# Optimization experiments

Hardware: AMD Instinct MI355X
Metric: run time of the kernel (lower is better)

## Reference

```python
import jax, jax.numpy as jnp
import numpy as np

NUM_HEADS = 8
DIM = 256
HEAD_DIM = DIM // NUM_HEADS  # 32
CPB_HIDDEN = 512
FFN_HIDDEN = 1024


def _relative_position_cpb(query_size, key_size, pretrain_size):
    # TransNeXt-style continuous position bias table + index (query==key grid here)
    qh, qw = query_size
    kh, kw = key_size
    ph, pw = pretrain_size
    aqh = np.arange(qh, dtype=np.float64)
    akh = np.arange(kh, dtype=np.float64)
    aqw = np.arange(qw, dtype=np.float64)
    akw = np.arange(kw, dtype=np.float64)
    kH, kW = np.meshgrid(akh, akw, indexing='ij')
    qH, qW = np.meshgrid(aqh, aqw, indexing='ij')
    rel_h = (qH.reshape(-1)[:, None] - kH.reshape(-1)[None, :]) / (ph - 1) * 8.0
    rel_w = (qW.reshape(-1)[:, None] - kW.reshape(-1)[None, :]) / (pw - 1) * 8.0
    rel = np.stack([rel_h, rel_w], axis=-1).reshape(-1, 2)
    table, idx = np.unique(rel, return_inverse=True, axis=0)
    table = np.sign(table) * np.log2(np.abs(table) + 1.0) / np.log2(8.0)
    return idx.astype(np.int32).reshape(-1), table.astype(np.float32)


def setup_inputs() -> dict:
    key = jax.random.key(0)
    ks = jax.random.split(key, 16)
    B, C, H, W = 8, 256, 128, 128
    q = jax.random.normal(ks[0], (B, C, H, W), dtype=jnp.float32)
    kv = jax.random.normal(ks[1], (B, C, H, W), dtype=jnp.float32)
    rel_idx_np, rel_table_np = _relative_position_cpb((32, 32), (32, 32), (32, 32))
    s = 0.02
    inp = {
        'q': q,
        'kv': kv,
        'rel_pos_index': jnp.asarray(rel_idx_np),
        'rel_coords_table': jnp.asarray(rel_table_np),
        'Wq': jax.random.normal(ks[2], (DIM, DIM), jnp.float32) * s,
        'bq': jnp.zeros((DIM,), jnp.float32),
        'Wkv': jax.random.normal(ks[3], (DIM, 2 * DIM), jnp.float32) * s,
        'bkv': jnp.zeros((2 * DIM,), jnp.float32),
        'Wo': jax.random.normal(ks[4], (DIM, DIM), jnp.float32) * s,
        'bo': jnp.zeros((DIM,), jnp.float32),
        'cpb_w1': jax.random.normal(ks[5], (2, CPB_HIDDEN), jnp.float32) * s,
        'cpb_b1': jnp.zeros((CPB_HIDDEN,), jnp.float32),
        'cpb_w2': jax.random.normal(ks[6], (CPB_HIDDEN, NUM_HEADS), jnp.float32) * s,
        'cpb_b2': jnp.zeros((NUM_HEADS,), jnp.float32),
        'ffn_w1': jax.random.normal(ks[7], (DIM, FFN_HIDDEN), jnp.float32) * s,
        'ffn_b1': jnp.zeros((FFN_HIDDEN,), jnp.float32),
        'ffn_w2': jax.random.normal(ks[8], (FFN_HIDDEN, DIM), jnp.float32) * s,
        'ffn_b2': jnp.zeros((DIM,), jnp.float32),
        'ln_g': jnp.ones((DIM,), jnp.float32),
        'ln_b': jnp.zeros((DIM,), jnp.float32),
    }
    return inp


def _resize_bilinear(x, size):
    # matches torch F.interpolate(mode='bilinear', align_corners=False)
    return jax.image.resize(x, (x.shape[0], x.shape[1], size[0], size[1]),
                            method='linear', antialias=False)


def _layernorm(x, g, b, eps=1e-5):
    mu = jnp.mean(x, axis=-1, keepdims=True)
    var = jnp.mean(jnp.square(x - mu), axis=-1, keepdims=True)
    return (x - mu) * jax.lax.rsqrt(var + eps) * g + b


def _fpn_forward(q, kv, rel_pos_index, rel_coords_table, Wq, bq, Wkv, bkv, Wo, bo,
                 cpb_w1, cpb_b1, cpb_w2, cpb_b2, ffn_w1, ffn_b1, ffn_w2, ffn_b2, ln_g, ln_b):
    x = q
    B, C, H, W = q.shape
    pH = H // 4
    pW = H // 4  # note: original code uses h for both, matching square inputs
    N = pH * pW

    qd = jax.nn.relu(_resize_bilinear(q, (pH, pW)))   # [B,C,pH,pW] (dropout p=0)
    kvd = jax.nn.relu(_resize_bilinear(kv, (pH, pW)))
    qt = qd.reshape(B, C, N).transpose(0, 2, 1)   # [B,N,C]
    kvt = kvd.reshape(B, C, N).transpose(0, 2, 1)  # [B,N,C]

    # --- BVAM: cross-attention with continuous relative position bias ---
    qh = (qt @ Wq + bq).reshape(B, N, NUM_HEADS, HEAD_DIM).transpose(0, 2, 1, 3)  # [B,h,N,d]
    kvp = (kvt @ Wkv + bkv).reshape(B, N, 2, NUM_HEADS, HEAD_DIM).transpose(2, 0, 3, 1, 4)
    k, v = kvp[0], kvp[1]  # [B,h,N,d]

    cpb = jax.nn.relu(rel_coords_table @ cpb_w1 + cpb_b1) @ cpb_w2 + cpb_b2  # [L,h]
    bias = cpb[rel_pos_index].reshape(N, N, NUM_HEADS).transpose(2, 0, 1)    # [h,N,N]

    scale = 1.0 / jnp.sqrt(jnp.float32(HEAD_DIM))
    logits = jnp.einsum('bhnd,bhmd->bhnm', qh, k) * scale + bias[None]
    attn = jax.nn.softmax(logits, axis=-1)
    out = jnp.einsum('bhnm,bhmd->bhnd', attn, v)
    out = out.transpose(0, 2, 1, 3).reshape(B, N, C) @ Wo + bo  # [B,N,C]

    # --- FFN (post-norm, gelu) ---
    ff = jax.nn.gelu(out @ ffn_w1 + ffn_b1, approximate=False) @ ffn_w2 + ffn_b2
    y = _layernorm(out + ff, ln_g, ln_b)  # [B,N,C]

    # back to spatial, upsample, residual
    y = y.transpose(0, 2, 1).reshape(B, C, pH, pW)
    y = jax.nn.relu(_resize_bilinear(y, (H, W)))
    return x + y


def reference(q, kv, rel_pos_index, rel_coords_table, Wq, bq, Wkv, bkv, Wo, bo,
              cpb_w1, cpb_b1, cpb_w2, cpb_b2, ffn_w1, ffn_b1, ffn_w2, ffn_b2, ln_g, ln_b):
    return _fpn_forward(q, kv, rel_pos_index, rel_coords_table, Wq, bq, Wkv, bkv, Wo, bo,
                        cpb_w1, cpb_b1, cpb_w2, cpb_b2, ffn_w1, ffn_b1, ffn_w2, ffn_b2, ln_g, ln_b)
```

## Files before the change

### kernel.cpp

```cpp
#include <hip/hip_runtime.h>
#include <hip/hip_bf16.h>
#include <hip/hip_fp16.h>

typedef __hip_bfloat16 bf16;
typedef __attribute__((ext_vector_type(8))) __bf16 bf16x8;
typedef __attribute__((ext_vector_type(4))) __bf16 bf16x4;
typedef __attribute__((ext_vector_type(4))) float f32x4;
typedef __attribute__((ext_vector_type(4))) float f4;

__device__ __forceinline__ void gload_lds16(const bf16* g, bf16* l)
{
    __builtin_amdgcn_global_load_lds((const __attribute__((address_space(1))) void*)g,
                                     (__attribute__((address_space(3))) void*)l, 16, 0, 0);
}

__global__ __launch_bounds__(256) void prep_kernel(
    const float* __restrict__ tab, const float* __restrict__ w1, const float* __restrict__ b1,
    const float* __restrict__ w2, const float* __restrict__ b2, float* __restrict__ cpbout, int L, int ncpb,
    const float* __restrict__ Wq, const float* __restrict__ Wkv, const float* __restrict__ Wo,
    const float* __restrict__ fw1, const float* __restrict__ fw2,
    bf16* __restrict__ WqT, bf16* __restrict__ WkvT, bf16* __restrict__ WoT,
    bf16* __restrict__ W1T, bf16* __restrict__ W2T,
    const float* __restrict__ qsrc, const float* __restrict__ kvsrc,
    bf16* __restrict__ qdst, bf16* __restrict__ kvdst)
{
    __shared__ float o[32][33];
    const int t = threadIdx.x;
    int bid = blockIdx.x;
    if (bid < ncpb) {
        int l = bid * 32 + (t >> 3);
        int js = t & 7;
        bool valid = l < L;
        float t0 = valid ? tab[2 * l] : 0.f, t1 = valid ? tab[2 * l + 1] : 0.f;
        float acc[8];
#pragma unroll
        for (int hh = 0; hh < 8; ++hh) acc[hh] = 0.f;
        for (int j = js; j < 512; j += 8) {
            float hv = fmaxf(t0 * w1[j] + t1 * w1[512 + j] + b1[j], 0.f);
            f4 w2a = *(const f4*)&w2[j * 8];
            f4 w2b = *(const f4*)&w2[j * 8 + 4];
#pragma unroll
            for (int hh = 0; hh < 4; ++hh) { acc[hh] += hv * w2a[hh]; acc[4 + hh] += hv * w2b[hh]; }
        }
#pragma unroll
        for (int d = 1; d < 8; d <<= 1)
#pragma unroll
            for (int hh = 0; hh < 8; ++hh) acc[hh] += __shfl_xor(acc[hh], d);
        if (js == 0 && valid)
#pragma unroll
            for (int hh = 0; hh < 8; ++hh) cpbout[(size_t)hh * L + l] = acc[hh] + b2[hh];
        return;
    }
    bid -= ncpb;
    if (bid < 3072) {
        const float* W; bf16* WT; int K, N, base;
        if (bid < 256)       { W = Wq;  WT = WqT;  K = 256;  N = 256;  base = 0; }
        else if (bid < 768)  { W = Wkv; WT = WkvT; K = 256;  N = 512;  base = 256; }
        else if (bid < 1024) { W = Wo;  WT = WoT;  K = 256;  N = 256;  base = 768; }
        else if (bid < 2048) { W = fw1; WT = W1T;  K = 256;  N = 1024; base = 1024; }
        else                 { W = fw2; WT = W2T;  K = 1024; N = 256;  base = 2048; }
        int idx = (bid - base) * 256 + t;
        int n = idx / K, k = idx % K;
        WT[idx] = (bf16)W[(size_t)k * N + n];
        return;
    }
    bid -= 3072;
    {
        const float* src = bid < 2048 ? qsrc : kvsrc;
        bf16* dst = bid < 2048 ? qdst : kvdst;
        int bb2 = bid & 2047;
        int cc = bb2 & 7, i = (bb2 >> 3) & 31, b = bb2 >> 8;
#pragma unroll
        for (int p = 0; p < 4; ++p) {
            int id = p * 256 + t;
            int c = id >> 5, j = id & 31;
            const float* r = src + ((size_t)(b * 256 + cc * 32 + c) * 128 + 4 * i + 1) * 128 + 4 * j;
            float4 r1 = *(const float4*)r;
            float4 r2 = *(const float4*)(r + 128);
            o[c][j] = 0.25f * (r1.y + r1.z + r2.y + r2.z);
        }
        __syncthreads();
#pragma unroll
        for (int p = 0; p < 4; ++p) {
            int id = p * 256 + t;
            int j = id >> 5, c = id & 31;
            dst[(size_t)(b * 1024 + i * 32 + j) * 256 + cc * 32 + c] = (bf16)fmaxf(o[c][j], 0.f);
        }
    }
}

__global__ __launch_bounds__(256) void bias_gather_kernel(
    const int* __restrict__ ridx, const float* __restrict__ cpbh,
    bf16* __restrict__ biasF, int L)
{
    __shared__ int rix[32][32];
    const int qt = blockIdx.x, mt = blockIdx.y;
    const int t = threadIdx.x;
    {
        int q = t >> 3, m4 = (t & 7) * 4;
        *(int4*)&rix[q][m4] = *(const int4*)&ridx[(size_t)(qt * 32 + q) * 1024 + mt * 32 + m4];
    }
    __syncthreads();
    const int ls = t & 63, qj = (t >> 6) & 1, hg = t >> 7;
    const int lo = ls & 15, hi = ls >> 4;
    int lidx[8];
#pragma unroll
    for (int j = 0; j < 8; ++j) {
        int kf = j >> 2, r = j & 3;
        lidx[j] = rix[qj * 16 + lo][kf * 16 + hi * 4 + r];
    }
#pragma unroll
    for (int hh = 0; hh < 4; ++hh) {
        int h = hg * 4 + hh;
        const float* ct = cpbh + (size_t)h * L;
        bf16 vals[8];
#pragma unroll
        for (int j = 0; j < 8; ++j) vals[j] = (bf16)ct[lidx[j]];
        size_t off = ((((size_t)(h * 32 + qt) * 32 + mt) * 2 + qj) * 64 + ls) * 8;
        *(bf16x8*)&biasF[off] = *(const bf16x8*)vals;
    }
}

template<int BM, int BN>
__device__ __forceinline__ void gemm_core(
    const bf16* __restrict__ A, const bf16* __restrict__ BT, int K,
    int m0, int n0, bf16* As, bf16* Bs, f32x4 (&acc)[BM / 32][BN / 32])
{
    constexpr int MI = BM / 32, NJ = BN / 32;
    const int tid = threadIdx.x;
    const int lane = tid & 63, wid = tid >> 6;
    const int lo = lane & 15, hi = lane >> 4;
    const int wr = wid >> 1, wc = wid & 1;
#pragma unroll
    for (int i = 0; i < MI; ++i)
#pragma unroll
        for (int j = 0; j < NJ; ++j) acc[i][j] = f32x4{0.f, 0.f, 0.f, 0.f};

    for (int k0 = 0; k0 < K; k0 += 64) {
        __syncthreads();
#pragma unroll
        for (int p = 0; p < BM / 32; ++p) {
            int f = p * 256 + wid * 64 + lane;
            int row = f >> 3, cs = f & 7;
            gload_lds16(&A[(size_t)(m0 + row) * K + k0 + ((cs ^ (row & 7)) * 8)],
                        As + (size_t)(p * 256 + wid * 64) * 8);
        }
#pragma unroll
        for (int p = 0; p < BN / 32; ++p) {
            int f = p * 256 + wid * 64 + lane;
            int row = f >> 3, cs = f & 7;
            gload_lds16(&BT[(size_t)(n0 + row) * K + k0 + ((cs ^ (row & 7)) * 8)],
                        Bs + (size_t)(p * 256 + wid * 64) * 8);
        }
        __syncthreads();
        bf16x8 af[2][MI], bfr[2][NJ];
#pragma unroll
        for (int kk = 0; kk < 2; ++kk) {
#pragma unroll
            for (int i = 0; i < MI; ++i) {
                int row = wr * (BM / 2) + i * 16 + lo;
                af[kk][i] = *(const bf16x8*)&As[row * 64 + (((kk * 4 + hi) ^ (lo & 7)) * 8)];
            }
#pragma unroll
            for (int j = 0; j < NJ; ++j) {
                int row = wc * (BN / 2) + j * 16 + lo;
                bfr[kk][j] = *(const bf16x8*)&Bs[row * 64 + (((kk * 4 + hi) ^ (lo & 7)) * 8)];
            }
        }
#pragma unroll
        for (int kk = 0; kk < 2; ++kk)
#pragma unroll
            for (int i = 0; i < MI; ++i)
#pragma unroll
                for (int j = 0; j < NJ; ++j)
                    acc[i][j] = __builtin_amdgcn_mfma_f32_16x16x32_bf16(af[kk][i], bfr[kk][j], acc[i][j], 0, 0, 0);
    }
}

template<int BM, int BN>
__global__ __launch_bounds__(256) void gemm_bt(
    const bf16* __restrict__ A, const bf16* __restrict__ BT,
    const float* __restrict__ bias, bf16* __restrict__ Cb, float* __restrict__ Cf,
    const bf16* __restrict__ resid, int M, int N, int K, int act)
{
    constexpr int MI = BM / 32, NJ = BN / 32;
    __shared__ __align__(16) bf16 As[BM * 64];
    __shared__ __align__(16) bf16 Bs[BN * 64];
    const int tid = threadIdx.x;
    const int lane = tid & 63, wid = tid >> 6;
    const int lo = lane & 15, hi = lane >> 4;
    const int m0 = blockIdx.x * BM, n0 = blockIdx.y * BN;
    const int wr = wid >> 1, wc = wid & 1;
    f32x4 acc[MI][NJ];
    gemm_core<BM, BN>(A, BT, K, m0, n0, As, Bs, acc);
#pragma unroll
    for (int i = 0; i < MI; ++i)
#pragma unroll
        for (int j = 0; j < NJ; ++j) {
            int col = n0 + wc * (BN / 2) + j * 16 + lo;
            float bv = bias[col];
#pragma unroll
            for (int r = 0; r < 4; ++r) {
                int row = m0 + wr * (BM / 2) + i * 16 + hi * 4 + r;
                float v = acc[i][j][r] + bv;
                if (act == 1) v = 0.5f * v * (1.f + erff(v * 0.70710678118654752f));
                if (resid) v += (float)resid[(size_t)row * N + col];
                if (Cb) Cb[(size_t)row * N + col] = (bf16)v;
                else    Cf[(size_t)row * N + col] = v;
            }
        }
}

__global__ __launch_bounds__(256) void gemm_qkv(
    const bf16* __restrict__ qt, const bf16* __restrict__ WqT, const float* __restrict__ bq,
    bf16* __restrict__ qhb,
    const bf16* __restrict__ kvt, const bf16* __restrict__ WkvT, const float* __restrict__ bkv,
    bf16* __restrict__ kvpb, bf16* __restrict__ vT)
{
    __shared__ __align__(16) bf16 As[64 * 64];
    __shared__ __align__(16) bf16 Bs[64 * 64];
    const int tid = threadIdx.x;
    const int lane = tid & 63, wid = tid >> 6;
    const int lo = lane & 15, hi = lane >> 4;
    const int wr = wid >> 1, wc = wid & 1;
    const int by = blockIdx.y;
    const bf16 *A, *BT; const float* bias; int n0;
    if (by < 4)      { A = qt;  BT = WqT;  bias = bq;  n0 = by * 64; }
    else             { A = kvt; BT = WkvT; bias = bkv; n0 = (by - 4) * 64; }
    const int m0 = blockIdx.x * 64;
    f32x4 acc[2][2];
    gemm_core<64, 64>(A, BT, 256, m0, n0, As, Bs, acc);
#pragma unroll
    for (int i = 0; i < 2; ++i)
#pragma unroll
        for (int j = 0; j < 2; ++j) {
            int col = n0 + wc * 32 + j * 16 + lo;
            float bv = bias[col];
            if (by < 4) {
#pragma unroll
                for (int r = 0; r < 4; ++r) {
                    int row = m0 + wr * 32 + i * 16 + hi * 4 + r;
                    qhb[(size_t)row * 256 + col] = (bf16)(acc[i][j][r] + bv);
                }
            } else if (by < 8) {
#pragma unroll
                for (int r = 0; r < 4; ++r) {
                    int row = m0 + wr * 32 + i * 16 + hi * 4 + r;
                    kvpb[(size_t)row * 512 + col] = (bf16)(acc[i][j][r] + bv);
                }
            } else {
                int vcol = col - 256;
                int h = vcol >> 5, d = vcol & 31;
                int b = m0 >> 10;
                int mbase = (m0 & 1023) + wr * 32 + i * 16 + hi * 4;
                bf16 tmp[4];
#pragma unroll
                for (int r = 0; r < 4; ++r) tmp[r] = (bf16)(acc[i][j][r] + bv);
                *(bf16x4*)&vT[(size_t)((b * 8 + h) * 32 + d) * 1024 + mbase] = *(const bf16x4*)tmp;
            }
        }
}

__global__ __launch_bounds__(256) void ffn2_ln_kernel(
    const bf16* __restrict__ A, const bf16* __restrict__ BT,
    const float* __restrict__ bias, const bf16* __restrict__ resid,
    const float* __restrict__ g, const float* __restrict__ bb,
    bf16* __restrict__ ysp)
{
    __shared__ __align__(16) bf16 As[32 * 64];
    __shared__ __align__(16) bf16 Bs[256 * 64];
    __shared__ float buf[32][260];
    const int tid = threadIdx.x;
    const int lane = tid & 63, wid = tid >> 6;
    const int lo = lane & 15, hi = lane >> 4;
    const int m0 = blockIdx.x * 32;
    f32x4 acc[2][4];
#pragma unroll
    for (int i = 0; i < 2; ++i)
#pragma unroll
        for (int j = 0; j < 4; ++j) acc[i][j] = f32x4{0.f, 0.f, 0.f, 0.f};

    for (int k0 = 0; k0 < 1024; k0 += 64) {
        __syncthreads();
        {
            int f = tid, row = f >> 3, cs = f & 7;
            gload_lds16(&A[(size_t)(m0 + row) * 1024 + k0 + ((cs ^ (row & 7)) * 8)],
                        As + (size_t)(wid * 64) * 8);
        }
#pragma unroll
        for (int p = 0; p < 8; ++p) {
            int f = p * 256 + tid, row = f >> 3, cs = f & 7;
            gload_lds16(&BT[(size_t)row * 1024 + k0 + ((cs ^ (row & 7)) * 8)],
                        Bs + (size_t)(p * 256 + wid * 64) * 8);
        }
        __syncthreads();
        bf16x8 af[2][2], bfr[2][4];
#pragma unroll
        for (int kk = 0; kk < 2; ++kk) {
#pragma unroll
            for (int i = 0; i < 2; ++i) {
                int row = i * 16 + lo;
                af[kk][i] = *(const bf16x8*)&As[row * 64 + (((kk * 4 + hi) ^ (lo & 7)) * 8)];
            }
#pragma unroll
            for (int j = 0; j < 4; ++j) {
                int row = wid * 64 + j * 16 + lo;
                bfr[kk][j] = *(const bf16x8*)&Bs[row * 64 + (((kk * 4 + hi) ^ (lo & 7)) * 8)];
            }
        }
#pragma unroll
        for (int kk = 0; kk < 2; ++kk)
#pragma unroll
            for (int i = 0; i < 2; ++i)
#pragma unroll
                for (int j = 0; j < 4; ++j)
                    acc[i][j] = __builtin_amdgcn_mfma_f32_16x16x32_bf16(af[kk][i], bfr[kk][j], acc[i][j], 0, 0, 0);
    }
#pragma unroll
    for (int i = 0; i < 2; ++i)
#pragma unroll
        for (int j = 0; j < 4; ++j) {
            int col = wid * 64 + j * 16 + lo;
            float bv = bias[col];
#pragma unroll
            for (int r = 0; r < 4; ++r) {
                int lr = i * 16 + hi * 4 + r;
                buf[lr][col] = acc[i][j][r] + bv + (float)resid[(size_t)(m0 + lr) * 256 + col];
            }
        }
    __syncthreads();
#pragma unroll
    for (int rr = 0; rr < 8; ++rr) {
        int row = wid * 8 + rr;
        f4 x = *(const f4*)&buf[row][lane * 4];
        float s = x[0] + x[1] + x[2] + x[3];
#pragma unroll
        for (int d = 1; d < 64; d <<= 1) s += __shfl_xor(s, d);
        float mean = s * (1.f / 256.f);
        f4 dv = {x[0] - mean, x[1] - mean, x[2] - mean, x[3] - mean};
        float s2 = dv[0] * dv[0] + dv[1] * dv[1] + dv[2] * dv[2] + dv[3] * dv[3];
#pragma unroll
        for (int d = 1; d < 64; d <<= 1) s2 += __shfl_xor(s2, d);
        float rstd = rsqrtf(s2 * (1.f / 256.f) + 1e-5f);
        f4 o = {dv[0] * rstd, dv[1] * rstd, dv[2] * rstd, dv[3] * rstd};
        *(f4*)&buf[row][lane * 4] = o;
    }
    __syncthreads();
    float gc = g[tid], bc = bb[tid];
    int b = m0 >> 10, n0l = m0 & 1023;
    bf16* dst = &ysp[((size_t)(b * 256 + tid) << 10) + n0l];
#pragma unroll
    for (int p = 0; p < 4; ++p) {
        bf16 tmp[8];
#pragma unroll
        for (int k = 0; k < 8; ++k) tmp[k] = (bf16)(buf[p * 8 + k][tid] * gc + bc);
        *(bf16x8*)&dst[p * 8] = *(const bf16x8*)tmp;
    }
}

__global__ __launch_bounds__(256) void attn_kernel(
    const bf16* __restrict__ qh, const bf16* __restrict__ kvp, const bf16* __restrict__ vT,
    const bf16* __restrict__ biasF, bf16* __restrict__ attnout)
{
    __shared__ __align__(16) bf16 Ps[4][32 * 40];
    __shared__ __align__(16) __half accs[4][32][34];
    __shared__ float pm[4][32], pl[4][32];
    const int tid = threadIdx.x, lane = tid & 63, wid = tid >> 6;
    const int lo = lane & 15, hi = lane >> 4;
    const int qt = blockIdx.x, n0 = qt * 32;
    const int h = blockIdx.y;
    const int b = blockIdx.z;
    const float scale = 0.17677669529663687f;
    const f32x4 zero4 = {0.f, 0.f, 0.f, 0.f};

    bf16x8 qf[2];
#pragma unroll
    for (int qj = 0; qj < 2; ++qj)
        qf[qj] = *(const bf16x8*)&qh[(size_t)(b * 1024 + n0 + qj * 16 + lo) * 256 + h * 32 + hi * 8];

    f32x4 acc[2][2];
#pragma unroll
    for (int i = 0; i < 2; ++i)
#pragma unroll
        for (int j = 0; j < 2; ++j) acc[i][j] = zero4;
    float mrow[2] = {-1e30f, -1e30f}, lrow[2] = {0.f, 0.f};

    bf16* Pw = Ps[wid];

    for (int t = wid; t < 32; t += 4) {
        const int m0 = t * 32;
        bf16x8 kfr0 = *(const bf16x8*)&kvp[(size_t)(b * 1024 + m0 + lo) * 512 + h * 32 + hi * 8];
        bf16x8 kfr1 = *(const bf16x8*)&kvp[(size_t)(b * 1024 + m0 + 16 + lo) * 512 + h * 32 + hi * 8];
        bf16x8 va0 = *(const bf16x8*)&vT[(size_t)((b * 8 + h) * 32 + lo) * 1024 + m0 + hi * 8];
        bf16x8 va1 = *(const bf16x8*)&vT[(size_t)((b * 8 + h) * 32 + 16 + lo) * 1024 + m0 + hi * 8];
        size_t boff = (((size_t)(h * 32 + qt) * 32 + t) * 2 * 64 + lane) * 8;
        bf16x8 bv0 = *(const bf16x8*)&biasF[boff];
        bf16x8 bv1 = *(const bf16x8*)&biasF[boff + 512];

        f32x4 s[2][2];
        s[0][0] = __builtin_amdgcn_mfma_f32_16x16x32_bf16(kfr0, qf[0], zero4, 0, 0, 0);
        s[0][1] = __builtin_amdgcn_mfma_f32_16x16x32_bf16(kfr0, qf[1], zero4, 0, 0, 0);
        s[1][0] = __builtin_amdgcn_mfma_f32_16x16x32_bf16(kfr1, qf[0], zero4, 0, 0, 0);
        s[1][1] = __builtin_amdgcn_mfma_f32_16x16x32_bf16(kfr1, qf[1], zero4, 0, 0, 0);
#pragma unroll
        for (int kf = 0; kf < 2; ++kf)
#pragma unroll
            for (int r = 0; r < 4; ++r) {
                s[kf][0][r] = s[kf][0][r] * scale + (float)bv0[kf * 4 + r];
                s[kf][1][r] = s[kf][1][r] * scale + (float)bv1[kf * 4 + r];
            }
#pragma unroll
        for (int qj = 0; qj < 2; ++qj) {
            float mx = fmaxf(fmaxf(fmaxf(s[0][qj][0], s[0][qj][1]), fmaxf(s[0][qj][2], s[0][qj][3])),
                             fmaxf(fmaxf(s[1][qj][0], s[1][qj][1]), fmaxf(s[1][qj][2], s[1][qj][3])));
            mx = fmaxf(mx, __shfl_xor(mx, 16));
            mx = fmaxf(mx, __shfl_xor(mx, 32));
            float mnew = fmaxf(mrow[qj], mx);
            float alpha = __expf(mrow[qj] - mnew);
            float rs = 0.f;
#pragma unroll
            for (int kf = 0; kf < 2; ++kf)
#pragma unroll
                for (int r = 0; r < 4; ++r) {
                    float p = __expf(s[kf][qj][r] - mnew);
                    s[kf][qj][r] = p;
                    rs += p;
                }
            rs += __shfl_xor(rs, 16);
            rs += __shfl_xor(rs, 32);
            lrow[qj] = lrow[qj] * alpha + rs;
            mrow[qj] = mnew;
#pragma unroll
            for (int di = 0; di < 2; ++di)
#pragma unroll
                for (int r = 0; r < 4; ++r) acc[di][qj][r] *= alpha;
        }
#pragma unroll
        for (int qj = 0; qj < 2; ++qj)
#pragma unroll
            for (int kf = 0; kf < 2; ++kf)
#pragma unroll
                for (int r = 0; r < 4; ++r)
                    Pw[(qj * 16 + lo) * 40 + kf * 16 + hi * 4 + r] = (bf16)s[kf][qj][r];
        bf16x8 pb0 = *(const bf16x8*)&Pw[lo * 40 + hi * 8];
        bf16x8 pb1 = *(const bf16x8*)&Pw[(16 + lo) * 40 + hi * 8];
        acc[0][0] = __builtin_amdgcn_mfma_f32_16x16x32_bf16(va0, pb0, acc[0][0], 0, 0, 0);
        acc[0][1] = __builtin_amdgcn_mfma_f32_16x16x32_bf16(va0, pb1, acc[0][1], 0, 0, 0);
        acc[1][0] = __builtin_amdgcn_mfma_f32_16x16x32_bf16(va1, pb0, acc[1][0], 0, 0, 0);
        acc[1][1] = __builtin_amdgcn_mfma_f32_16x16x32_bf16(va1, pb1, acc[1][1], 0, 0, 0);
    }
#pragma unroll
    for (int di = 0; di < 2; ++di)
#pragma unroll
        for (int qj = 0; qj < 2; ++qj)
#pragma unroll
            for (int r = 0; r < 4; ++r)
                accs[wid][di * 16 + hi * 4 + r][qj * 16 + lo] = __float2half(acc[di][qj][r]);
    if (hi == 0) {
#pragma unroll
        for (int qj = 0; qj < 2; ++qj) {
            pm[wid][qj * 16 + lo] = mrow[qj];
            pl[wid][qj * 16 + lo] = lrow[qj];
        }
    }
    __syncthreads();
    int q = tid >> 3, d0 = (tid & 7) * 4;
    float M = fmaxf(fmaxf(pm[0][q], pm[1][q]), fmaxf(pm[2][q], pm[3][q]));
    float f0 = __expf(pm[0][q] - M), f1 = __expf(pm[1][q] - M);
    float f2 = __expf(pm[2][q] - M), f3 = __expf(pm[3][q] - M);
    float inv = 1.f / (pl[0][q] * f0 + pl[1][q] * f1 + pl[2][q] * f2 + pl[3][q] * f3);
    bf16 tmp[4];
#pragma unroll
    for (int j = 0; j < 4; ++j) {
        int d = d0 + j;
        float o = f0 * (float)accs[0][d][q] + f1 * (float)accs[1][d][q] +
                  f2 * (float)accs[2][d][q] + f3 * (float)accs[3][d][q];
        tmp[j] = (bf16)(o * inv);
    }
    *(bf16x4*)&attnout[(size_t)(b * 1024 + n0 + q) * 256 + h * 32 + d0] = *(const bf16x4*)tmp;
}

__global__ __launch_bounds__(256) void upsample_kernel(const float* __restrict__ x,
    const bf16* __restrict__ ysp, float* __restrict__ out)
{
    int idx = blockIdx.x * 256 + threadIdx.x;
    int w4 = idx & 31; int r1 = idx >> 5;
    int hh = r1 & 127; int r2 = r1 >> 7;
    int c = r2 & 255; int b = r2 >> 8;
    float chh = 0.25f * hh - 0.375f;
    float fi = floorf(chh);
    float fh = chh - fi;
    int i0 = (int)fi;
    int ia = i0 < 0 ? 0 : i0;
    int ib = (i0 + 1) > 31 ? 31 : (i0 + 1);
    const bf16* yr = ysp + ((size_t)(b * 256 + c) << 10);
    const bf16* ra = yr + ia * 32;
    const bf16* rb = yr + ib * 32;
    f4 xv = *(const f4*)&x[(size_t)idx * 4];
    f4 o;
#pragma unroll
    for (int k = 0; k < 4; ++k) {
        int ww = w4 * 4 + k;
        float cww = 0.25f * ww - 0.375f;
        float fj = floorf(cww);
        float fw = cww - fj;
        int j0 = (int)fj;
        int ja = j0 < 0 ? 0 : j0;
        int jb = (j0 + 1) > 31 ? 31 : (j0 + 1);
        float v = (1.f - fh) * ((1.f - fw) * (float)ra[ja] + fw * (float)ra[jb]) +
                  fh * ((1.f - fw) * (float)rb[ja] + fw * (float)rb[jb]);
        o[k] = xv[k] + fmaxf(v, 0.f);
    }
    *(f4*)&out[(size_t)idx * 4] = o;
}

extern "C" void kernel_launch(void* const* d_in, const int* in_sizes, int n_in,
                              void* d_out, int out_size, void* d_ws, size_t ws_size,
                              hipStream_t stream)
{
    (void)n_in; (void)out_size; (void)ws_size;
    const float* q    = (const float*)d_in[0];
    const float* kv   = (const float*)d_in[1];
    const int*   ridx = (const int*)d_in[2];
    const float* rtab = (const float*)d_in[3];
    const float* Wq   = (const float*)d_in[4];
    const float* bq   = (const float*)d_in[5];
    const float* Wkv  = (const float*)d_in[6];
    const float* bkv  = (const float*)d_in[7];
    const float* Wo   = (const float*)d_in[8];
    const float* bo   = (const float*)d_in[9];
    const float* cw1  = (const float*)d_in[10];
    const float* cb1  = (const float*)d_in[11];
    const float* cw2  = (const float*)d_in[12];
    const float* cb2  = (const float*)d_in[13];
    const float* fw1  = (const float*)d_in[14];
    const float* fb1  = (const float*)d_in[15];
    const float* fw2  = (const float*)d_in[16];
    const float* fb2  = (const float*)d_in[17];
    const float* lng  = (const float*)d_in[18];
    const float* lnb  = (const float*)d_in[19];
    const int L = in_sizes[3] / 2;
    const int ncpb = (L + 31) / 32;

    char* w = (char*)d_ws;
    auto alloc = [&](size_t bytes) { char* p = w; w += (bytes + 255) & ~(size_t)255; return p; };
    bf16* qt      = (bf16*)alloc(8192ull * 256 * 2);
    bf16* kvt     = (bf16*)alloc(8192ull * 256 * 2);
    bf16* qhb     = (bf16*)alloc(8192ull * 256 * 2);
    bf16* kvpb    = (bf16*)alloc(8192ull * 512 * 2);
    bf16* vTb     = (bf16*)alloc(8ull * 8 * 32 * 1024 * 2);
    bf16* attnb   = (bf16*)alloc(8192ull * 256 * 2);
    bf16* outb    = (bf16*)alloc(8192ull * 256 * 2);
    bf16* ffh     = (bf16*)alloc(8192ull * 1024 * 2);
    bf16* ysp     = (bf16*)alloc(8ull * 256 * 1024 * 2);
    bf16* WqT     = (bf16*)alloc(256ull * 256 * 2);
    bf16* WkvT    = (bf16*)alloc(512ull * 256 * 2);
    bf16* WoT     = (bf16*)alloc(256ull * 256 * 2);
    bf16* W1T     = (bf16*)alloc(1024ull * 256 * 2);
    bf16* W2T     = (bf16*)alloc(256ull * 1024 * 2);
    float* cpbb   = (float*)alloc((size_t)8 * L * 4);
    bf16* biasF   = ffh;

    prep_kernel<<<dim3(ncpb + 3072 + 4096), 256, 0, stream>>>(
        rtab, cw1, cb1, cw2, cb2, cpbb, L, ncpb,
        Wq, Wkv, Wo, fw1, fw2, WqT, WkvT, WoT, W1T, W2T,
        q, kv, qt, kvt);
    bias_gather_kernel<<<dim3(32, 32), 256, 0, stream>>>(ridx, cpbb, biasF, L);
    gemm_qkv<<<dim3(128, 12), 256, 0, stream>>>(qt, WqT, bq, qhb, kvt, WkvT, bkv, kvpb, vTb);
    attn_kernel<<<dim3(32, 8, 8), 256, 0, stream>>>(qhb, kvpb, vTb, biasF, attnb);
    gemm_bt<64, 64><<<dim3(128, 4), 256, 0, stream>>>(attnb, WoT, bo, outb, nullptr, nullptr, 8192, 256, 256, 0);
    gemm_bt<128, 64><<<dim3(64, 16), 256, 0, stream>>>(outb, W1T, fb1, ffh, nullptr, nullptr, 8192, 1024, 256, 1);
    ffn2_ln_kernel<<<dim3(256), 256, 0, stream>>>(ffh, W2T, fb2, outb, lng, lnb, ysp);
    upsample_kernel<<<dim3(32768), 256, 0, stream>>>(q, ysp, (float*)d_out);
}
```

Before: 190.5 us.

## Fuse bias gather into QKV GEMM, tile weight transposes, shrink FFN2 tiles

Weight transposes in the prep kernel now go through a 32x32 shared-memory tile, so reads are coalesced and writes are vectorised, replacing the earlier strided per-element transpose. The pooled-input store is vectorised to bf16x4. The bias gather kernel is folded into the QKV GEMM launch as extra grid rows, which removes one launch. The FFN2+LayerNorm kernel drops from 32-row to 16-row tiles so it gets 512 blocks instead of 256, raising occupancy at the cost of reloading the W2 tiles more often.

```diff
diff --git a/kernel.cpp b/kernel.cpp
--- a/kernel.cpp
+++ b/kernel.cpp
@@ -52,19 +52,31 @@
         return;
     }
     bid -= ncpb;
-    if (bid < 3072) {
+    if (bid < 768) {
         const float* W; bf16* WT; int K, N, base;
-        if (bid < 256)       { W = Wq;  WT = WqT;  K = 256;  N = 256;  base = 0; }
-        else if (bid < 768)  { W = Wkv; WT = WkvT; K = 256;  N = 512;  base = 256; }
-        else if (bid < 1024) { W = Wo;  WT = WoT;  K = 256;  N = 256;  base = 768; }
-        else if (bid < 2048) { W = fw1; WT = W1T;  K = 256;  N = 1024; base = 1024; }
-        else                 { W = fw2; WT = W2T;  K = 1024; N = 256;  base = 2048; }
-        int idx = (bid - base) * 256 + t;
-        int n = idx / K, k = idx % K;
-        WT[idx] = (bf16)W[(size_t)k * N + n];
+        if (bid < 64)        { W = Wq;  WT = WqT;  K = 256;  N = 256;  base = 0; }
+        else if (bid < 192)  { W = Wkv; WT = WkvT; K = 256;  N = 512;  base = 64; }
+        else if (bid < 256)  { W = Wo;  WT = WoT;  K = 256;  N = 256;  base = 192; }
+        else if (bid < 512)  { W = fw1; WT = W1T;  K = 256;  N = 1024; base = 256; }
+        else                 { W = fw2; WT = W2T;  K = 1024; N = 256;  base = 512; }
+        int lid = bid - base;
+        int tn = N >> 5;
+        int k0 = (lid / tn) << 5, n0 = (lid % tn) << 5;
+        {
+            int r = t >> 3, cc = (t & 7) * 4;
+            *(f4*)&o[r][cc] = *(const f4*)&W[(size_t)(k0 + r) * N + n0 + cc];
+        }
+        __syncthreads();
+        {
+            int n = t >> 3, kk = (t & 7) * 4;
+            bf16 tmp[4];
+#pragma unroll
+            for (int i = 0; i < 4; ++i) tmp[i] = (bf16)o[kk + i][n];
+            *(bf16x4*)&WT[(size_t)(n0 + n) * K + k0 + kk] = *(const bf16x4*)tmp;
+        }
         return;
     }
-    bid -= 3072;
+    bid -= 768;
     {
         const float* src = bid < 2048 ? qsrc : kvsrc;
         bf16* dst = bid < 2048 ? qdst : kvdst;
@@ -80,44 +92,13 @@
             o[c][j] = 0.25f * (r1.y + r1.z + r2.y + r2.z);
         }
         __syncthreads();
-#pragma unroll
-        for (int p = 0; p < 4; ++p) {
-            int id = p * 256 + t;
-            int j = id >> 5, c = id & 31;
-            dst[(size_t)(b * 1024 + i * 32 + j) * 256 + cc * 32 + c] = (bf16)fmaxf(o[c][j], 0.f);
-        }
-    }
-}
-
-__global__ __launch_bounds__(256) void bias_gather_kernel(
-    const int* __restrict__ ridx, const float* __restrict__ cpbh,
-    bf16* __restrict__ biasF, int L)
-{
-    __shared__ int rix[32][32];
-    const int qt = blockIdx.x, mt = blockIdx.y;
-    const int t = threadIdx.x;
-    {
-        int q = t >> 3, m4 = (t & 7) * 4;
-        *(int4*)&rix[q][m4] = *(const int4*)&ridx[(size_t)(qt * 32 + q) * 1024 + mt * 32 + m4];
-    }
-    __syncthreads();
-    const int ls = t & 63, qj = (t >> 6) & 1, hg = t >> 7;
-    const int lo = ls & 15, hi = ls >> 4;
-    int lidx[8];
-#pragma unroll
-    for (int j = 0; j < 8; ++j) {
-        int kf = j >> 2, r = j & 3;
-        lidx[j] = rix[qj * 16 + lo][kf * 16 + hi * 4 + r];
-    }
-#pragma unroll
-    for (int hh = 0; hh < 4; ++hh) {
-        int h = hg * 4 + hh;
-        const float* ct = cpbh + (size_t)h * L;
-        bf16 vals[8];
-#pragma unroll
-        for (int j = 0; j < 8; ++j) vals[j] = (bf16)ct[lidx[j]];
-        size_t off = ((((size_t)(h * 32 + qt) * 32 + mt) * 2 + qj) * 64 + ls) * 8;
-        *(bf16x8*)&biasF[off] = *(const bf16x8*)vals;
+        {
+            int j = t >> 3, c4 = (t & 7) * 4;
+            bf16 tmp[4];
+#pragma unroll
+            for (int k = 0; k < 4; ++k) tmp[k] = (bf16)fmaxf(o[c4 + k][j], 0.f);
+            *(bf16x4*)&dst[(size_t)(b * 1024 + i * 32 + j) * 256 + cc * 32 + c4] = *(const bf16x4*)tmp;
+        }
     }
 }
 
@@ -215,15 +196,45 @@
     const bf16* __restrict__ qt, const bf16* __restrict__ WqT, const float* __restrict__ bq,
     bf16* __restrict__ qhb,
     const bf16* __restrict__ kvt, const bf16* __restrict__ WkvT, const float* __restrict__ bkv,
-    bf16* __restrict__ kvpb, bf16* __restrict__ vT)
+    bf16* __restrict__ kvpb, bf16* __restrict__ vT,
+    const int* __restrict__ ridx, const float* __restrict__ cpbh,
+    bf16* __restrict__ biasF, int L)
 {
     __shared__ __align__(16) bf16 As[64 * 64];
     __shared__ __align__(16) bf16 Bs[64 * 64];
     const int tid = threadIdx.x;
     const int lane = tid & 63, wid = tid >> 6;
     const int lo = lane & 15, hi = lane >> 4;
+    const int by = blockIdx.y;
+    if (by >= 12) {
+        __shared__ int rix[32][32];
+        int id = (by - 12) * 128 + blockIdx.x;
+        int qtb = id >> 5, mt = id & 31;
+        {
+            int q = tid >> 3, m4 = (tid & 7) * 4;
+            *(int4*)&rix[q][m4] = *(const int4*)&ridx[(size_t)(qtb * 32 + q) * 1024 + mt * 32 + m4];
+        }
+        __syncthreads();
+        const int qj = (tid >> 6) & 1, hg = tid >> 7;
+        int lidx[8];
+#pragma unroll
+        for (int j = 0; j < 8; ++j) {
+            int kf = j >> 2, r = j & 3;
+            lidx[j] = rix[qj * 16 + lo][kf * 16 + hi * 4 + r];
+        }
+#pragma unroll
+        for (int hh = 0; hh < 4; ++hh) {
+            int h = hg * 4 + hh;
+            const float* ct = cpbh + (size_t)h * L;
+            bf16 vals[8];
+#pragma unroll
+            for (int j = 0; j < 8; ++j) vals[j] = (bf16)ct[lidx[j]];
+            size_t off = ((((size_t)(h * 32 + qtb) * 32 + mt) * 2 + qj) * 64 + lane) * 8;
+            *(bf16x8*)&biasF[off] = *(const bf16x8*)vals;
+        }
+        return;
+    }
     const int wr = wid >> 1, wc = wid & 1;
-    const int by = blockIdx.y;
     const bf16 *A, *BT; const float* bias; int n0;
     if (by < 4)      { A = qt;  BT = WqT;  bias = bq;  n0 = by * 64; }
     else             { A = kvt; BT = WkvT; bias = bkv; n0 = (by - 4) * 64; }
@@ -267,23 +278,21 @@
     const float* __restrict__ g, const float* __restrict__ bb,
     bf16* __restrict__ ysp)
 {
-    __shared__ __align__(16) bf16 As[32 * 64];
+    __shared__ __align__(16) bf16 As[16 * 64];
     __shared__ __align__(16) bf16 Bs[256 * 64];
-    __shared__ float buf[32][260];
+    __shared__ float buf[16][260];
     const int tid = threadIdx.x;
     const int lane = tid & 63, wid = tid >> 6;
     const int lo = lane & 15, hi = lane >> 4;
-    const int m0 = blockIdx.x * 32;
-    f32x4 acc[2][4];
-#pragma unroll
-    for (int i = 0; i < 2; ++i)
-#pragma unroll
-        for (int j = 0; j < 4; ++j) acc[i][j] = f32x4{0.f, 0.f, 0.f, 0.f};
+    const int m0 = blockIdx.x * 16;
+    f32x4 acc[4];
+#pragma unroll
+    for (int j = 0; j < 4; ++j) acc[j] = f32x4{0.f, 0.f, 0.f, 0.f};
 
     for (int k0 = 0; k0 < 1024; k0 += 64) {
         __syncthreads();
-        {
-            int f = tid, row = f >> 3, cs = f & 7;
+        if (tid < 128) {
+            int row = tid >> 3, cs = tid & 7;
             gload_lds16(&A[(size_t)(m0 + row) * 1024 + k0 + ((cs ^ (row & 7)) * 8)],
                         As + (size_t)(wid * 64) * 8);
         }
@@ -294,14 +303,10 @@
                         Bs + (size_t)(p * 256 + wid * 64) * 8);
         }
         __syncthreads();
-        bf16x8 af[2][2], bfr[2][4];
+        bf16x8 af[2], bfr[2][4];
 #pragma unroll
         for (int kk = 0; kk < 2; ++kk) {
-#pragma unroll
-            for (int i = 0; i < 2; ++i) {
-                int row = i * 16 + lo;
-                af[kk][i] = *(const bf16x8*)&As[row * 64 + (((kk * 4 + hi) ^ (lo & 7)) * 8)];
-            }
+            af[kk] = *(const bf16x8*)&As[lo * 64 + (((kk * 4 + hi) ^ (lo & 7)) * 8)];
 #pragma unroll
             for (int j = 0; j < 4; ++j) {
                 int row = wid * 64 + j * 16 + lo;
@@ -311,27 +316,23 @@
 #pragma unroll
         for (int kk = 0; kk < 2; ++kk)
 #pragma unroll
-            for (int i = 0; i < 2; ++i)
-#pragma unroll
-                for (int j = 0; j < 4; ++j)
-                    acc[i][j] = __builtin_amdgcn_mfma_f32_16x16x32_bf16(af[kk][i], bfr[kk][j], acc[i][j], 0, 0, 0);
-    }
-#pragma unroll
-    for (int i = 0; i < 2; ++i)
-#pragma unroll
-        for (int j = 0; j < 4; ++j) {
-            int col = wid * 64 + j * 16 + lo;
-            float bv = bias[col];
-#pragma unroll
-            for (int r = 0; r < 4; ++r) {
-                int lr = i * 16 + hi * 4 + r;
-                buf[lr][col] = acc[i][j][r] + bv + (float)resid[(size_t)(m0 + lr) * 256 + col];
-            }
-        }
+            for (int j = 0; j < 4; ++j)
+                acc[j] = __builtin_amdgcn_mfma_f32_16x16x32_bf16(af[kk], bfr[kk][j], acc[j], 0, 0, 0);
+    }
+#pragma unroll
+    for (int j = 0; j < 4; ++j) {
+        int col = wid * 64 + j * 16 + lo;
+        float bv = bias[col];
+#pragma unroll
+        for (int r = 0; r < 4; ++r) {
+            int lr = hi * 4 + r;
+            buf[lr][col] = acc[j][r] + bv + (float)resid[(size_t)(m0 + lr) * 256 + col];
+        }
+    }
     __syncthreads();
 #pragma unroll
-    for (int rr = 0; rr < 8; ++rr) {
-        int row = wid * 8 + rr;
+    for (int rr = 0; rr < 4; ++rr) {
+        int row = wid * 4 + rr;
         f4 x = *(const f4*)&buf[row][lane * 4];
         float s = x[0] + x[1] + x[2] + x[3];
 #pragma unroll
@@ -350,7 +351,7 @@
     int b = m0 >> 10, n0l = m0 & 1023;
     bf16* dst = &ysp[((size_t)(b * 256 + tid) << 10) + n0l];
 #pragma unroll
-    for (int p = 0; p < 4; ++p) {
+    for (int p = 0; p < 2; ++p) {
         bf16 tmp[8];
 #pragma unroll
         for (int k = 0; k < 8; ++k) tmp[k] = (bf16)(buf[p * 8 + k][tid] * gc + bc);
@@ -561,15 +562,15 @@
     float* cpbb   = (float*)alloc((size_t)8 * L * 4);
     bf16* biasF   = ffh;
 
-    prep_kernel<<<dim3(ncpb + 3072 + 4096), 256, 0, stream>>>(
+    prep_kernel<<<dim3(ncpb + 768 + 4096), 256, 0, stream>>>(
         rtab, cw1, cb1, cw2, cb2, cpbb, L, ncpb,
         Wq, Wkv, Wo, fw1, fw2, WqT, WkvT, WoT, W1T, W2T,
         q, kv, qt, kvt);
-    bias_gather_kernel<<<dim3(32, 32), 256, 0, stream>>>(ridx, cpbb, biasF, L);
-    gemm_qkv<<<dim3(128, 12), 256, 0, stream>>>(qt, WqT, bq, qhb, kvt, WkvT, bkv, kvpb, vTb);
+    gemm_qkv<<<dim3(128, 20), 256, 0, stream>>>(qt, WqT, bq, qhb, kvt, WkvT, bkv, kvpb, vTb,
+                                                ridx, cpbb, biasF, L);
     attn_kernel<<<dim3(32, 8, 8), 256, 0, stream>>>(qhb, kvpb, vTb, biasF, attnb);
     gemm_bt<64, 64><<<dim3(128, 4), 256, 0, stream>>>(attnb, WoT, bo, outb, nullptr, nullptr, 8192, 256, 256, 0);
     gemm_bt<128, 64><<<dim3(64, 16), 256, 0, stream>>>(outb, W1T, fb1, ffh, nullptr, nullptr, 8192, 1024, 256, 1);
-    ffn2_ln_kernel<<<dim3(256), 256, 0, stream>>>(ffh, W2T, fb2, outb, lng, lnb, ysp);
+    ffn2_ln_kernel<<<dim3(512), 256, 0, stream>>>(ffh, W2T, fb2, outb, lng, lnb, ysp);
     upsample_kernel<<<dim3(32768), 256, 0, stream>>>(q, ysp, (float*)d_out);
 }
```

New measurement: 189.2 us (median of 2 runs). Within noise of the previous version (-0.7%).
